# Performance work log

Hardware: AMD Instinct MI355X
Metric: run time of the kernel (lower is better)

The kernel has to match this reference:

```python
import jax, jax.numpy as jnp
import numpy as np

H, HK, D, W = 16, 4, 128, 512   # heads, kv heads, head dim, window size
SCALE = D ** -0.5
T = 8192


def setup_inputs() -> dict:
    key = jax.random.key(0)
    k1, k2, k3 = jax.random.split(key, 3)
    return {
        "query": jax.random.normal(k1, (T, H * D), dtype=jnp.float32),
        "key": jax.random.normal(k2, (T, HK * D), dtype=jnp.float32),
        "value": jax.random.normal(k3, (T, HK * D), dtype=jnp.float32),
    }


def reference(query, key, value):
    """Causal sliding-window attention (window W, incl. self) returning (out, lse).

    Banded formulation: queries are split into blocks of size W; each block
    attends only to its own block and the previous block, so the full [T,T]
    score matrix is never materialized.
    """
    Tn = query.shape[0]
    nb = Tn // W
    G = H // HK  # query heads per kv head
    q = query.reshape(nb, W, HK, G, D)
    k = key.reshape(nb, W, HK, D)
    v = value.reshape(nb, W, HK, D)
    # previous block of keys/values (zeros before block 0, masked out below)
    k_prev = jnp.concatenate([jnp.zeros_like(k[:1]), k[:-1]], axis=0)
    v_prev = jnp.concatenate([jnp.zeros_like(v[:1]), v[:-1]], axis=0)
    kk = jnp.concatenate([k_prev, k], axis=1)  # [nb, 2W, HK, D]
    vv = jnp.concatenate([v_prev, v], axis=1)
    # scores: [nb, HK, G, W, 2W]
    s = jnp.einsum('nqhgd,nkhd->nhgqk', q, kk) * SCALE
    i = jnp.arange(W)[:, None]       # local query pos
    j = jnp.arange(2 * W)[None, :]   # local key pos; key_abs - q_abs = j - W - i
    in_win = (j >= i + 1) & (j <= i + W)        # W keys ending at self
    b_idx = jnp.arange(nb)[:, None, None]
    valid = in_win[None] & ((b_idx > 0) | (j[None] >= W))  # block 0 has no prev keys
    s = jnp.where(valid[:, None, None], s, jnp.finfo(s.dtype).min)
    s32 = s.astype(jnp.float32)
    lse = jax.nn.logsumexp(s32, axis=-1)          # [nb, HK, G, W]
    p = jnp.exp(s32 - lse[..., None]).astype(q.dtype)
    o = jnp.einsum('nhgqk,nkhd->nqhgd', p, vv)
    out = o.reshape(Tn, H * D)
    lse_out = lse.transpose(1, 2, 0, 3).reshape(H, Tn)  # head h = hk*G + g
    return out, lse_out
```

## Files before the change

kernel.cpp:

```cpp
#include <hip/hip_runtime.h>
#include <hip/hip_bf16.h>


#define T_SEQ 8192
#define H_Q   16
#define HK_KV 4
#define D_HD  128
#define W_WIN 512
#define SCL2E 0.12753785397738803f
#define LN2   0.6931471805599453f

typedef __bf16 bf16_t;
typedef bf16_t bf16x8 __attribute__((ext_vector_type(8)));
typedef float  f32x4  __attribute__((ext_vector_type(4)));
typedef ushort us8    __attribute__((ext_vector_type(8)));

union U4 { uint2 u; bf16_t b[4]; };

__device__ inline bf16x8 to_bf8(float4 a, float4 b) {
    bf16x8 r;
    r[0] = (bf16_t)a.x; r[1] = (bf16_t)a.y; r[2] = (bf16_t)a.z; r[3] = (bf16_t)a.w;
    r[4] = (bf16_t)b.x; r[5] = (bf16_t)b.y; r[6] = (bf16_t)b.z; r[7] = (bf16_t)b.w;
    return r;
}

__device__ __forceinline__ void gld16(const void* g, void* l) {
    __builtin_amdgcn_global_load_lds(
        (const __attribute__((address_space(1))) void*)g,
        (__attribute__((address_space(3))) void*)l, 16, 0, 0);
}

__global__ __launch_bounds__(256) void prep_k(const float* __restrict__ key,
                                              bf16_t* __restrict__ Kb) {
    int e = (blockIdx.x * 256 + threadIdx.x) * 4;
    int t  = e >> 9;
    int c  = e & 511;
    int hk = c >> 7;
    int d  = c & 127;
    float4 v = *(const float4*)(key + e);
    U4 p;
    p.b[0] = (bf16_t)v.x; p.b[1] = (bf16_t)v.y; p.b[2] = (bf16_t)v.z; p.b[3] = (bf16_t)v.w;
    *(uint2*)(void*)(Kb + ((size_t)hk * T_SEQ + t) * 128 + d) = p.u;
}

__global__ __launch_bounds__(256) void prep_v(const float* __restrict__ val,
                                              bf16_t* __restrict__ Vt) {
    __shared__ ushort tile[64][68];
    int b   = blockIdx.x;
    int hk  = b >> 8;
    int rem = b & 255;
    int t0  = (rem & 127) << 6;
    int d0  = (rem >> 7) << 6;
    int tid = threadIdx.x;

    int i  = tid >> 2;
    int j0 = (tid & 3) << 4;
    const float* src = val + (size_t)(t0 + i) * 512 + hk * 128 + d0 + j0;
#pragma unroll
    for (int k = 0; k < 4; ++k) {
        float4 v = *(const float4*)(src + 4 * k);
        U4 p;
        p.b[0] = (bf16_t)v.x; p.b[1] = (bf16_t)v.y; p.b[2] = (bf16_t)v.z; p.b[3] = (bf16_t)v.w;
        *(uint2*)(void*)&tile[i][j0 + 4 * k] = p.u;
    }
    __syncthreads();
    int dd8 = tid >> 3;
    int tq  = (tid & 7) << 3;
#pragma unroll
    for (int half = 0; half < 2; ++half) {
        int dd = half * 32 + dd8;
        us8 u;
#pragma unroll
        for (int j = 0; j < 8; ++j) u[j] = tile[tq + j][dd];
        bf16_t* dst = Vt + ((size_t)hk * 128 + d0 + dd) * T_SEQ + t0 + tq;
        *(us8*)(void*)dst = u;
    }
}

__global__ __launch_bounds__(256) void attn_main(const float* __restrict__ qg,
                                                 const bf16_t* __restrict__ Kb,
                                                 const bf16_t* __restrict__ Vt,
                                                 float* __restrict__ out) {
    __shared__ ushort Kls[2][4096] __attribute__((aligned(16)));
    __shared__ ushort Vls[2][4096] __attribute__((aligned(16)));
    __shared__ ushort Plds[4][16][40] __attribute__((aligned(16)));

    const int bid = blockIdx.x;
    const int w   = (bid & 7) * 256 + (bid >> 3);
    const int h   = w >> 7;
    const int qb  = w & 127;
    const int hk  = h >> 2;
    const int tid  = threadIdx.x;
    const int wv   = tid >> 6;
    const int lane = tid & 63;
    const int lq   = lane & 15;
    const int g    = lane >> 4;
    const int q0b  = qb * 64;
    const int q0w  = q0b + wv * 16;
    const int qa   = q0w + lq;

    bf16x8 qf[4];
    const float* qp = qg + (size_t)qa * 2048 + h * 128 + 8 * g;
#pragma unroll
    for (int kc = 0; kc < 4; ++kc) {
        float4 a = *(const float4*)(qp + kc * 32);
        float4 b = *(const float4*)(qp + kc * 32 + 4);
        qf[kc] = to_bf8(a, b);
    }

    f32x4 acc[8];
#pragma unroll
    for (int i = 0; i < 8; ++i) acc[i] = (f32x4){0.f, 0.f, 0.f, 0.f};
    float mrun = -1e4f;
    float lsum = 0.f;

    const bf16_t* kb_ = Kb + (size_t)hk * T_SEQ * 128;
    const bf16_t* vb_ = Vt + (size_t)hk * 128 * T_SEQ;

    const int lob  = q0b - (W_WIN - 1);
    const int ktb0 = lob > 0 ? (lob >> 5) : 0;
    const int ktb1 = (q0b + 63) >> 5;
    const int wlow = q0w - (W_WIN - 1);

    auto stage = [&](int bf, int kbs) {
#pragma unroll
        for (int is = 0; is < 2; ++is) {
            int slot = is * 256 + tid;
            int krow = slot >> 4;
            int kch  = (slot & 15) ^ (krow & 7);
            gld16(kb_ + (size_t)(kbs + krow) * 128 + kch * 8,
                  (char*)&Kls[bf][0] + slot * 16);
        }
#pragma unroll
        for (int is = 0; is < 2; ++is) {
            int slot = is * 256 + tid;
            int vrow = slot >> 2;
            int vch  = (slot & 3) ^ ((vrow >> 1) & 3);
            gld16(vb_ + (size_t)vrow * T_SEQ + kbs + vch * 8,
                  (char*)&Vls[bf][0] + slot * 16);
        }
    };

    int buf = 0;
    stage(0, ktb0 << 5);
    asm volatile("s_waitcnt vmcnt(0)" ::: "memory");
    __syncthreads();

    for (int kt = ktb0; kt <= ktb1; ++kt) {
        const int kbs = kt << 5;
        if (kt < ktb1) stage(buf ^ 1, (kt + 1) << 5);

        if (kbs + 31 >= wlow && kbs <= q0w + 15) {
            f32x4 s0 = {0.f, 0.f, 0.f, 0.f}, s1 = {0.f, 0.f, 0.f, 0.f};
            const char* kb0  = (const char*)&Kls[buf][0] + lq * 256;
            const int   kxor = (lq & 7) << 4;
#pragma unroll
            for (int kc = 0; kc < 4; ++kc) {
                int cb = kc * 64 + g * 16;
                bf16x8 k0 = *(const bf16x8*)(kb0 + (cb ^ kxor));
                bf16x8 k1 = *(const bf16x8*)(kb0 + 4096 + (cb ^ kxor));
                s0 = __builtin_amdgcn_mfma_f32_16x16x32_bf16(k0, qf[kc], s0, 0, 0, 0);
                s1 = __builtin_amdgcn_mfma_f32_16x16x32_bf16(k1, qf[kc], s1, 0, 0, 0);
            }

            float sv[8];
#pragma unroll
            for (int r = 0; r < 4; ++r) {
                int kv0 = kbs + 4 * g + r;
                int kv1 = kv0 + 16;
                sv[r]     = (kv0 >= qa - (W_WIN - 1) && kv0 <= qa) ? s0[r] * SCL2E : -1e30f;
                sv[4 + r] = (kv1 >= qa - (W_WIN - 1) && kv1 <= qa) ? s1[r] * SCL2E : -1e30f;
            }

            float tmax = sv[0];
#pragma unroll
            for (int i = 1; i < 8; ++i) tmax = fmaxf(tmax, sv[i]);
            tmax = fmaxf(tmax, __shfl_xor(tmax, 16));
            tmax = fmaxf(tmax, __shfl_xor(tmax, 32));

            if (!__all(tmax <= mrun + 11.54f)) {
                float mnew  = fmaxf(mrun, tmax);
                float alpha = exp2f(mrun - mnew);
                lsum *= alpha;
#pragma unroll
                for (int i = 0; i < 8; ++i) acc[i] *= alpha;
                mrun = mnew;
            }

            float p[8];
            float psum = 0.f;
#pragma unroll
            for (int i = 0; i < 8; ++i) { p[i] = exp2f(sv[i] - mrun); psum += p[i]; }
            psum += __shfl_xor(psum, 16);
            psum += __shfl_xor(psum, 32);
            lsum += psum;

            U4 w0, w1;
            w0.b[0] = (bf16_t)p[0]; w0.b[1] = (bf16_t)p[1]; w0.b[2] = (bf16_t)p[2]; w0.b[3] = (bf16_t)p[3];
            w1.b[0] = (bf16_t)p[4]; w1.b[1] = (bf16_t)p[5]; w1.b[2] = (bf16_t)p[6]; w1.b[3] = (bf16_t)p[7];
            *(uint2*)(void*)&Plds[wv][lq][4 * g]      = w0.u;
            *(uint2*)(void*)&Plds[wv][lq][16 + 4 * g] = w1.u;
            asm volatile("s_waitcnt lgkmcnt(0)" ::: "memory");
            bf16x8 pb = *(const bf16x8*)(void*)&Plds[wv][lq][8 * g];

            const char* vb0 = (const char*)&Vls[buf][0] + lq * 64
                            + ((g ^ ((lq >> 1) & 3)) << 4);
#pragma unroll
            for (int dt = 0; dt < 8; ++dt) {
                bf16x8 vf = *(const bf16x8*)(vb0 + dt * 1024);
                acc[dt] = __builtin_amdgcn_mfma_f32_16x16x32_bf16(vf, pb, acc[dt], 0, 0, 0);
            }
        }

        asm volatile("s_waitcnt vmcnt(0)" ::: "memory");
        __syncthreads();
        buf ^= 1;
    }

    float inv = 1.0f / lsum;
#pragma unroll
    for (int dt = 0; dt < 8; ++dt) {
        float4 o;
        o.x = acc[dt][0] * inv; o.y = acc[dt][1] * inv;
        o.z = acc[dt][2] * inv; o.w = acc[dt][3] * inv;
        *(float4*)(out + (size_t)qa * 2048 + h * 128 + dt * 16 + 4 * g) = o;
    }
    if (lane < 16) {
        out[(size_t)T_SEQ * 2048 + (size_t)h * T_SEQ + qa] =
            LN2 * (mrun + log2f(lsum));
    }
}

extern "C" void kernel_launch(void* const* d_in, const int* in_sizes, int n_in,
                              void* d_out, int out_size, void* d_ws, size_t ws_size,
                              hipStream_t stream) {
    const float* q = (const float*)d_in[0];
    const float* k = (const float*)d_in[1];
    const float* v = (const float*)d_in[2];
    float* out = (float*)d_out;

    bf16_t* Kb = (bf16_t*)d_ws;
    bf16_t* Vt = Kb + (size_t)HK_KV * T_SEQ * D_HD;

    prep_k<<<(T_SEQ * HK_KV * D_HD) / (256 * 4), 256, 0, stream>>>(k, Kb);
    prep_v<<<HK_KV * (T_SEQ / 64) * (D_HD / 64), 256, 0, stream>>>(v, Vt);
    attn_main<<<(T_SEQ / 64) * H_Q, 256, 0, stream>>>(q, Kb, Vt, out);
}
```

Before: 222.9 us.

## Unroll attention K/V loop over static double buffers and fuse prep kernels

Merges the K and V bf16 prep kernels into a single launch to save one kernel launch. The main loop is unrolled by two over fixed LDS buffers, with global and LDS addresses precomputed outside the loop. The explicit vmcnt wait before each barrier is removed. Masking is skipped for fully interior tiles, the softmax scale is applied after the row max, exp2 uses the hardware builtin, and setprio wraps the MFMA sections. Dropping the explicit vmcnt wait risks reading LDS before the async global-to-LDS copy has landed, unless the compiler inserts the wait itself.

Measured after the change: 209.9 us. -5.8%, faster.

```diff
diff --git a/kernel.cpp b/kernel.cpp
--- a/kernel.cpp
+++ b/kernel.cpp
@@ -30,28 +30,29 @@
         (__attribute__((address_space(3))) void*)l, 16, 0, 0);
 }
 
-__global__ __launch_bounds__(256) void prep_k(const float* __restrict__ key,
-                                              bf16_t* __restrict__ Kb) {
-    int e = (blockIdx.x * 256 + threadIdx.x) * 4;
-    int t  = e >> 9;
-    int c  = e & 511;
-    int hk = c >> 7;
-    int d  = c & 127;
-    float4 v = *(const float4*)(key + e);
-    U4 p;
-    p.b[0] = (bf16_t)v.x; p.b[1] = (bf16_t)v.y; p.b[2] = (bf16_t)v.z; p.b[3] = (bf16_t)v.w;
-    *(uint2*)(void*)(Kb + ((size_t)hk * T_SEQ + t) * 128 + d) = p.u;
-}
-
-__global__ __launch_bounds__(256) void prep_v(const float* __restrict__ val,
-                                              bf16_t* __restrict__ Vt) {
+__global__ __launch_bounds__(256) void prep_kv(const float* __restrict__ key,
+                                               const float* __restrict__ val,
+                                               bf16_t* __restrict__ Kb,
+                                               bf16_t* __restrict__ Vt) {
     __shared__ ushort tile[64][68];
-    int b   = blockIdx.x;
+    const int tid = threadIdx.x;
+    if (blockIdx.x < 4096) {
+        int e = ((int)blockIdx.x * 256 + tid) * 4;
+        int t  = e >> 9;
+        int c  = e & 511;
+        int hk = c >> 7;
+        int d  = c & 127;
+        float4 v = *(const float4*)(key + e);
+        U4 p;
+        p.b[0] = (bf16_t)v.x; p.b[1] = (bf16_t)v.y; p.b[2] = (bf16_t)v.z; p.b[3] = (bf16_t)v.w;
+        *(uint2*)(void*)(Kb + ((size_t)hk * T_SEQ + t) * 128 + d) = p.u;
+        return;
+    }
+    int b   = blockIdx.x - 4096;
     int hk  = b >> 8;
     int rem = b & 255;
     int t0  = (rem & 127) << 6;
     int d0  = (rem >> 7) << 6;
-    int tid = threadIdx.x;
 
     int i  = tid >> 2;
     int j0 = (tid & 3) << 4;
@@ -121,101 +122,126 @@
     const int ktb0 = lob > 0 ? (lob >> 5) : 0;
     const int ktb1 = (q0b + 63) >> 5;
     const int wlow = q0w - (W_WIN - 1);
-
-    auto stage = [&](int bf, int kbs) {
-#pragma unroll
-        for (int is = 0; is < 2; ++is) {
-            int slot = is * 256 + tid;
-            int krow = slot >> 4;
-            int kch  = (slot & 15) ^ (krow & 7);
-            gld16(kb_ + (size_t)(kbs + krow) * 128 + kch * 8,
-                  (char*)&Kls[bf][0] + slot * 16);
-        }
-#pragma unroll
-        for (int is = 0; is < 2; ++is) {
-            int slot = is * 256 + tid;
-            int vrow = slot >> 2;
-            int vch  = (slot & 3) ^ ((vrow >> 1) & 3);
-            gld16(vb_ + (size_t)vrow * T_SEQ + kbs + vch * 8,
-                  (char*)&Vls[bf][0] + slot * 16);
-        }
+    const int bq   = 4 * g - qa + 511;
+
+    const uint okg0 = ((uint)(tid >> 4)) * 128 + (uint)(((tid & 15) ^ ((tid >> 4) & 7)) << 3);
+    const uint ovg0 = ((uint)(tid >> 2)) * T_SEQ + (uint)(((tid & 3) ^ ((tid >> 3) & 3)) << 3);
+    char* const ldsK0 = (char*)&Kls[0][0] + tid * 16;
+    char* const ldsK1 = (char*)&Kls[1][0] + tid * 16;
+    char* const ldsV0 = (char*)&Vls[0][0] + tid * 16;
+    char* const ldsV1 = (char*)&Vls[1][0] + tid * 16;
+
+    const uint e6  = (lane & 4) << 4;
+    const uint blo = (uint)((g * 16) ^ ((lq & 3) << 4));
+    const char* kbA_e = (const char*)&Kls[0][0] + lq * 256 + blo + e6;
+    const char* kbA_o = (const char*)&Kls[0][0] + lq * 256 + blo + (64 - e6);
+    const char* kbB_e = (const char*)&Kls[1][0] + lq * 256 + blo + e6;
+    const char* kbB_o = (const char*)&Kls[1][0] + lq * 256 + blo + (64 - e6);
+    const uint vswz = (uint)((g ^ ((lq >> 1) & 3)) << 4);
+    const char* vbA = (const char*)&Vls[0][0] + lq * 64 + vswz;
+    const char* vbB = (const char*)&Vls[1][0] + lq * 64 + vswz;
+
+    ushort* const pw0 = &Plds[wv][lq][4 * g];
+    ushort* const pw1 = pw0 + 16;
+    const ushort* const prd = &Plds[wv][lq][8 * g];
+
+    auto stage = [&](char* lk, char* lv, int kbs_) {
+        const bf16_t* kt_ = kb_ + (size_t)kbs_ * 128;
+        const bf16_t* vt_ = vb_ + kbs_;
+        gld16(kt_ + okg0,          lk);
+        gld16(kt_ + 2048 + okg0,   lk + 4096);
+        gld16(vt_ + ovg0,          lv);
+        gld16(vt_ + 524288 + ovg0, lv + 4096);
     };
 
-    int buf = 0;
-    stage(0, ktb0 << 5);
-    asm volatile("s_waitcnt vmcnt(0)" ::: "memory");
+    auto compute = [&](const char* kbe, const char* kbo, const char* vbp, int kbs_) {
+        if (kbs_ + 31 < wlow || kbs_ > q0w + 15) return;
+
+        f32x4 s0 = {0.f, 0.f, 0.f, 0.f}, s1 = {0.f, 0.f, 0.f, 0.f};
+        __builtin_amdgcn_s_setprio(1);
+#pragma unroll
+        for (int kc = 0; kc < 4; ++kc) {
+            const char* pa = (kc & 1) ? kbo : kbe;
+            const int  off = (kc >> 1) * 128;
+            bf16x8 k0 = *(const bf16x8*)(pa + off);
+            bf16x8 k1 = *(const bf16x8*)(pa + off + 4096);
+            s0 = __builtin_amdgcn_mfma_f32_16x16x32_bf16(k0, qf[kc], s0, 0, 0, 0);
+            s1 = __builtin_amdgcn_mfma_f32_16x16x32_bf16(k1, qf[kc], s1, 0, 0, 0);
+        }
+        __builtin_amdgcn_s_setprio(0);
+
+        float sv[8];
+        const bool interior = (kbs_ >= q0w - 496) && (kbs_ + 31 <= q0w);
+        if (interior) {
+#pragma unroll
+            for (int r = 0; r < 4; ++r) { sv[r] = s0[r]; sv[4 + r] = s1[r]; }
+        } else {
+            const int b0 = kbs_ + bq;
+#pragma unroll
+            for (int r = 0; r < 4; ++r) {
+                sv[r]     = ((uint)(b0 + r)      <= 511u) ? s0[r] : -1e30f;
+                sv[4 + r] = ((uint)(b0 + 16 + r) <= 511u) ? s1[r] : -1e30f;
+            }
+        }
+
+        float tm = sv[0];
+#pragma unroll
+        for (int i = 1; i < 8; ++i) tm = fmaxf(tm, sv[i]);
+        tm = fmaxf(tm, __shfl_xor(tm, 16));
+        tm = fmaxf(tm, __shfl_xor(tm, 32));
+        const float tms = tm * SCL2E;
+
+        if (!__all(tms <= mrun + 11.54f)) {
+            float mnew  = fmaxf(mrun, tms);
+            float alpha = __builtin_amdgcn_exp2f(mrun - mnew);
+            lsum *= alpha;
+#pragma unroll
+            for (int i = 0; i < 8; ++i) acc[i] *= alpha;
+            mrun = mnew;
+        }
+
+        float p[8];
+        float ps = 0.f;
+#pragma unroll
+        for (int i = 0; i < 8; ++i) {
+            p[i] = __builtin_amdgcn_exp2f(fmaf(sv[i], SCL2E, -mrun));
+            ps += p[i];
+        }
+        ps += __shfl_xor(ps, 16);
+        ps += __shfl_xor(ps, 32);
+        lsum += ps;
+
+        U4 w0, w1;
+        w0.b[0] = (bf16_t)p[0]; w0.b[1] = (bf16_t)p[1]; w0.b[2] = (bf16_t)p[2]; w0.b[3] = (bf16_t)p[3];
+        w1.b[0] = (bf16_t)p[4]; w1.b[1] = (bf16_t)p[5]; w1.b[2] = (bf16_t)p[6]; w1.b[3] = (bf16_t)p[7];
+        *(uint2*)(void*)pw0 = w0.u;
+        *(uint2*)(void*)pw1 = w1.u;
+        asm volatile("s_waitcnt lgkmcnt(0)" ::: "memory");
+        bf16x8 pb = *(const bf16x8*)(const void*)prd;
+
+        __builtin_amdgcn_s_setprio(1);
+#pragma unroll
+        for (int dt = 0; dt < 8; ++dt) {
+            bf16x8 vf = *(const bf16x8*)(vbp + dt * 1024);
+            acc[dt] = __builtin_amdgcn_mfma_f32_16x16x32_bf16(vf, pb, acc[dt], 0, 0, 0);
+        }
+        __builtin_amdgcn_s_setprio(0);
+    };
+
+    stage(ldsK0, ldsV0, ktb0 << 5);
     __syncthreads();
 
-    for (int kt = ktb0; kt <= ktb1; ++kt) {
-        const int kbs = kt << 5;
-        if (kt < ktb1) stage(buf ^ 1, (kt + 1) << 5);
-
-        if (kbs + 31 >= wlow && kbs <= q0w + 15) {
-            f32x4 s0 = {0.f, 0.f, 0.f, 0.f}, s1 = {0.f, 0.f, 0.f, 0.f};
-            const char* kb0  = (const char*)&Kls[buf][0] + lq * 256;
-            const int   kxor = (lq & 7) << 4;
-#pragma unroll
-            for (int kc = 0; kc < 4; ++kc) {
-                int cb = kc * 64 + g * 16;
-                bf16x8 k0 = *(const bf16x8*)(kb0 + (cb ^ kxor));
-                bf16x8 k1 = *(const bf16x8*)(kb0 + 4096 + (cb ^ kxor));
-                s0 = __builtin_amdgcn_mfma_f32_16x16x32_bf16(k0, qf[kc], s0, 0, 0, 0);
-                s1 = __builtin_amdgcn_mfma_f32_16x16x32_bf16(k1, qf[kc], s1, 0, 0, 0);
-            }
-
-            float sv[8];
-#pragma unroll
-            for (int r = 0; r < 4; ++r) {
-                int kv0 = kbs + 4 * g + r;
-                int kv1 = kv0 + 16;
-                sv[r]     = (kv0 >= qa - (W_WIN - 1) && kv0 <= qa) ? s0[r] * SCL2E : -1e30f;
-                sv[4 + r] = (kv1 >= qa - (W_WIN - 1) && kv1 <= qa) ? s1[r] * SCL2E : -1e30f;
-            }
-
-            float tmax = sv[0];
-#pragma unroll
-            for (int i = 1; i < 8; ++i) tmax = fmaxf(tmax, sv[i]);
-            tmax = fmaxf(tmax, __shfl_xor(tmax, 16));
-            tmax = fmaxf(tmax, __shfl_xor(tmax, 32));
-
-            if (!__all(tmax <= mrun + 11.54f)) {
-                float mnew  = fmaxf(mrun, tmax);
-                float alpha = exp2f(mrun - mnew);
-                lsum *= alpha;
-#pragma unroll
-                for (int i = 0; i < 8; ++i) acc[i] *= alpha;
-                mrun = mnew;
-            }
-
-            float p[8];
-            float psum = 0.f;
-#pragma unroll
-            for (int i = 0; i < 8; ++i) { p[i] = exp2f(sv[i] - mrun); psum += p[i]; }
-            psum += __shfl_xor(psum, 16);
-            psum += __shfl_xor(psum, 32);
-            lsum += psum;
-
-            U4 w0, w1;
-            w0.b[0] = (bf16_t)p[0]; w0.b[1] = (bf16_t)p[1]; w0.b[2] = (bf16_t)p[2]; w0.b[3] = (bf16_t)p[3];
-            w1.b[0] = (bf16_t)p[4]; w1.b[1] = (bf16_t)p[5]; w1.b[2] = (bf16_t)p[6]; w1.b[3] = (bf16_t)p[7];
-            *(uint2*)(void*)&Plds[wv][lq][4 * g]      = w0.u;
-            *(uint2*)(void*)&Plds[wv][lq][16 + 4 * g] = w1.u;
-            asm volatile("s_waitcnt lgkmcnt(0)" ::: "memory");
-            bf16x8 pb = *(const bf16x8*)(void*)&Plds[wv][lq][8 * g];
-
-            const char* vb0 = (const char*)&Vls[buf][0] + lq * 64
-                            + ((g ^ ((lq >> 1) & 3)) << 4);
-#pragma unroll
-            for (int dt = 0; dt < 8; ++dt) {
-                bf16x8 vf = *(const bf16x8*)(vb0 + dt * 1024);
-                acc[dt] = __builtin_amdgcn_mfma_f32_16x16x32_bf16(vf, pb, acc[dt], 0, 0, 0);
-            }
-        }
-
-        asm volatile("s_waitcnt vmcnt(0)" ::: "memory");
+    int kt = ktb0;
+    while (kt + 1 <= ktb1) {
+        stage(ldsK1, ldsV1, (kt + 1) << 5);
+        compute(kbA_e, kbA_o, vbA, kt << 5);
         __syncthreads();
-        buf ^= 1;
-    }
+        if (kt + 2 <= ktb1) stage(ldsK0, ldsV0, (kt + 2) << 5);
+        compute(kbB_e, kbB_o, vbB, (kt + 1) << 5);
+        __syncthreads();
+        kt += 2;
+    }
+    if (kt <= ktb1) compute(kbA_e, kbA_o, vbA, kt << 5);
 
     float inv = 1.0f / lsum;
 #pragma unroll
@@ -242,7 +268,6 @@
     bf16_t* Kb = (bf16_t*)d_ws;
     bf16_t* Vt = Kb + (size_t)HK_KV * T_SEQ * D_HD;
 
-    prep_k<<<(T_SEQ * HK_KV * D_HD) / (256 * 4), 256, 0, stream>>>(k, Kb);
-    prep_v<<<HK_KV * (T_SEQ / 64) * (D_HD / 64), 256, 0, stream>>>(v, Vt);
+    prep_kv<<<4096 + HK_KV * (T_SEQ / 64) * (D_HD / 64), 256, 0, stream>>>(k, v, Kb, Vt);
     attn_main<<<(T_SEQ / 64) * H_Q, 256, 0, stream>>>(q, Kb, Vt, out);
 }
```
